# Performance work log

Hardware: AMD Instinct MI355X
Metric: run time of the kernel (lower is better)

The kernel has to match this reference:

```python
import jax, jax.numpy as jnp
import numpy as np

B, C, H, W = 4, 256, 128, 128
K = 3
BN = max(16, C // 4)  # 64
PAD = K // 2
EPS = 1e-5


def conv2d(x, w, b=None, pad=0):
    out = jax.lax.conv_general_dilated(
        x, w, (1, 1), [(pad, pad), (pad, pad)],
        dimension_numbers=("NCHW", "OIHW", "NCHW"))
    if b is not None:
        out = out + b[None, :, None, None]
    return out


def deform_conv2d(z, offset, mask, w, b):
    # torchvision modulated deform conv v2: offset [B,2*K*K,H,W] interleaved (dy,dx),
    # mask [B,K*K,H,W], kernel positions row-major, stride 1, pad PAD.
    Bz, Cb, Hz, Wz = z.shape
    K2 = K * K
    off = offset.reshape(Bz, K2, 2, Hz, Wz)
    ky, kx = jnp.meshgrid(jnp.arange(K), jnp.arange(K), indexing="ij")
    # sampling positions py/px: [B, K2, H, W]
    py = off[:, :, 0] + jnp.arange(Hz)[None, None, :, None] + (ky.reshape(K2) - PAD)[None, :, None, None]
    px = off[:, :, 1] + jnp.arange(Wz)[None, None, None, :] + (kx.reshape(K2) - PAD)[None, :, None, None]
    y0 = jnp.floor(py)
    x0 = jnp.floor(px)
    wy1 = py - y0  # frac weights
    wx1 = px - x0
    z_flat = z.reshape(Bz, Cb, Hz * Wz)

    def gather(yy, xx, wgt):
        valid = (yy >= 0) & (yy < Hz) & (xx >= 0) & (xx < Wz)
        yc = jnp.clip(yy, 0, Hz - 1).astype(jnp.int32)
        xc = jnp.clip(xx, 0, Wz - 1).astype(jnp.int32)
        idx = (yc * Wz + xc).reshape(Bz, K2 * Hz * Wz)
        g = jnp.take_along_axis(z_flat, idx[:, None, :], axis=2)  # [B, Cb, K2*H*W]
        g = g.reshape(Bz, Cb, K2, Hz, Wz)
        return g * (wgt * valid.astype(z.dtype))[:, None]

    val = (gather(y0, x0, (1 - wy1) * (1 - wx1))
           + gather(y0, x0 + 1, (1 - wy1) * wx1)
           + gather(y0 + 1, x0, wy1 * (1 - wx1))
           + gather(y0 + 1, x0 + 1, wy1 * wx1))
    val = val * mask[:, None]  # modulate: [B, Cb, K2, H, W]
    out = jnp.einsum("bckhw,ock->bohw", val, w.reshape(w.shape[0], Cb, K2))
    return out + b[None, :, None, None]


def setup_inputs() -> dict:
    key = jax.random.key(0)
    ks = jax.random.split(key, 11)
    s = 0.05
    return {
        "x": jax.random.normal(ks[0], (B, C, H, W), jnp.float32),
        "down_w": jax.random.normal(ks[1], (BN, C, 1, 1), jnp.float32) * s,
        "off_w": jax.random.normal(ks[2], (2 * K * K, BN, 3, 3), jnp.float32) * s,
        "off_b": jax.random.normal(ks[3], (2 * K * K,), jnp.float32) * s,
        "mask_w": jax.random.normal(ks[4], (K * K, BN, 3, 3), jnp.float32) * s,
        "mask_b": jax.random.normal(ks[5], (K * K,), jnp.float32) * s,
        "def_w": jax.random.normal(ks[6], (BN, BN, K, K), jnp.float32) * s,
        "def_b": jax.random.normal(ks[7], (BN,), jnp.float32) * s,
        "up_w": jax.random.normal(ks[8], (C, BN, 1, 1), jnp.float32) * s,
        "gamma": jnp.ones((C,), jnp.float32),
        "beta": jnp.zeros((C,), jnp.float32),
    }


def reference(x, down_w, off_w, off_b, mask_w, mask_b, def_w, def_b, up_w, gamma, beta):
    z = conv2d(x, down_w)                               # 1x1 down: [B, BN, H, W]
    offset = conv2d(z, off_w, off_b, pad=1)             # [B, 18, H, W]
    mask = jax.nn.sigmoid(conv2d(z, mask_w, mask_b, pad=1))  # [B, 9, H, W]
    z = deform_conv2d(z, offset, mask, def_w, def_b)    # [B, BN, H, W]
    z = conv2d(z, up_w)                                 # 1x1 up: [B, C, H, W]
    y = x + z
    # BatchNorm2d in training mode: batch statistics over (B, H, W), biased var
    mean = jnp.mean(y, axis=(0, 2, 3), keepdims=True)
    var = jnp.var(y, axis=(0, 2, 3), keepdims=True)
    yh = (y - mean) * jax.lax.rsqrt(var + EPS)
    yh = yh * gamma[None, :, None, None] + beta[None, :, None, None]
    return yh * jax.nn.sigmoid(yh)  # SiLU
```

## Files before the change

kernel.cpp:

```cpp
#include <hip/hip_runtime.h>
#include <hip/hip_bf16.h>


typedef __attribute__((ext_vector_type(8))) short bf16x8;
typedef __attribute__((ext_vector_type(4))) short bf16x4;
typedef __attribute__((ext_vector_type(4))) float f32x4;

#define HW   16384
#define CC   256
#define BNC  64

#define WS_STATS   0
#define WS_SS      262144
#define WS_FD      264192
#define WS_FOM     296960
#define WS_FDEF    333824
#define WS_FUP     407552
#define WS_ZBF     440320
#define WS_OM      8828928

__device__ __forceinline__ short f2b(float f) {
    unsigned u = __float_as_uint(f);
    unsigned r = (u + 0x7FFFu + ((u >> 16) & 1u)) >> 16;
    return (short)r;
}
__device__ __forceinline__ float b2f(short s) {
    return __uint_as_float(((unsigned)(unsigned short)s) << 16);
}

__global__ void k_prep(const float* __restrict__ down_w, const float* __restrict__ off_w,
                       const float* __restrict__ mask_w, const float* __restrict__ def_w,
                       const float* __restrict__ up_w, char* __restrict__ ws) {
    int g = blockIdx.x * 256 + threadIdx.x;
    int row = g >> 6, lane = g & 63;
    if (row >= 172) return;
    int l15 = lane & 15, q = lane >> 4;
    short vals[8];
    short* dst;
    if (row < 32) {
        int nt = row >> 3, kk = row & 7;
        int n = nt * 16 + l15;
        for (int j = 0; j < 8; ++j) {
            int c = kk * 32 + q * 8 + j;
            vals[j] = f2b(down_w[n * 256 + c]);
        }
        dst = (short*)(ws + WS_FD) + row * 512 + lane * 8;
    } else if (row < 68) {
        int r = row - 32; int nt = r / 18, kk = r % 18;
        int n = nt * 16 + l15;
        for (int j = 0; j < 8; ++j) {
            int kap = kk * 32 + q * 8 + j; int k = kap >> 6, c = kap & 63;
            float v = 0.f;
            if (n < 18)      v = off_w[(n * 64 + c) * 9 + k];
            else if (n < 27) v = mask_w[((n - 18) * 64 + c) * 9 + k];
            vals[j] = f2b(v);
        }
        dst = (short*)(ws + WS_FOM) + r * 512 + lane * 8;
    } else if (row < 140) {
        int r = row - 68; int nt = r / 18, kk = r % 18;
        int n = nt * 16 + l15;
        int u = kk * 4 + q, k = u >> 3;
        for (int j = 0; j < 8; ++j) {
            int c = (u & 7) * 8 + j;
            vals[j] = f2b(def_w[(n * 64 + c) * 9 + k]);
        }
        dst = (short*)(ws + WS_FDEF) + r * 512 + lane * 8;
    } else {
        int r = row - 140; int nt = r >> 1, kk = r & 1;
        int o = nt * 16 + l15;
        for (int j = 0; j < 8; ++j) {
            int c = kk * 32 + q * 8 + j;
            vals[j] = f2b(up_w[o * 64 + c]);
        }
        dst = (short*)(ws + WS_FUP) + r * 512 + lane * 8;
    }
    for (int j = 0; j < 8; ++j) dst[j] = vals[j];
}

__global__ __launch_bounds__(256) void k_down(const float* __restrict__ x,
                                              const short* __restrict__ wfd,
                                              short* __restrict__ zbf) {
    __shared__ __align__(16) short xl[64 * 264];
    int blk = blockIdx.x;
    int b = blk >> 8;
    int hw0 = (blk & 255) * 64;
    int t = threadIdx.x;
    const float* xb = x + (size_t)b * CC * HW + hw0;
    int px = t & 63, w = t >> 6;
    for (int h = 0; h < 8; ++h) {
        int c0 = h * 32 + w * 8;
        bf16x8 pk;
        #pragma unroll
        for (int j = 0; j < 8; ++j)
            pk[j] = f2b(xb[(size_t)(c0 + j) * HW + px]);
        *(bf16x8*)(&xl[px * 264 + c0]) = pk;
    }
    __syncthreads();
    int lane = t & 63, wv = t >> 6;
    int l15 = lane & 15, q = lane >> 4;
    bf16x8 A[8];
    const short* xrow = &xl[(wv * 16 + l15) * 264];
    for (int kk = 0; kk < 8; ++kk)
        A[kk] = *(const bf16x8*)(xrow + kk * 32 + q * 8);
    const bf16x8* Bp = (const bf16x8*)wfd;
    size_t obase = ((size_t)b * HW + hw0 + wv * 16) * 64;
    for (int nt = 0; nt < 4; ++nt) {
        f32x4 acc = {0.f, 0.f, 0.f, 0.f};
        for (int kk = 0; kk < 8; ++kk) {
            bf16x8 Bf = Bp[(nt * 8 + kk) * 64 + lane];
            acc = __builtin_amdgcn_mfma_f32_16x16x32_bf16(A[kk], Bf, acc, 0, 0, 0);
        }
        int n = nt * 16 + l15;
        for (int r = 0; r < 4; ++r) {
            int prow = q * 4 + r;
            zbf[obase + (size_t)prow * 64 + n] = f2b(acc[r]);
        }
    }
}

__global__ __launch_bounds__(256) void k_offmask(const short* __restrict__ zbf,
                                                 const short* __restrict__ wfom,
                                                 const float* __restrict__ off_b,
                                                 const float* __restrict__ mask_b,
                                                 float* __restrict__ om) {
    int blk = blockIdx.x;
    int b = blk >> 8;
    int hw0 = (blk & 255) * 64;
    int y = hw0 >> 7, x0 = hw0 & 127;
    int t = threadIdx.x, lane = t & 63, wv = t >> 6;
    int l15 = lane & 15, q = lane >> 4;
    int xx0 = x0 + wv * 16 + l15;
    const short* zb = zbf + (size_t)b * HW * 64;
    f32x4 acc0 = {0, 0, 0, 0}, acc1 = {0, 0, 0, 0};
    const bf16x8* Bp = (const bf16x8*)wfom;
    for (int kk = 0; kk < 18; ++kk) {
        int k = kk >> 1;
        int yy = y + (k / 3) - 1;
        int xx = xx0 + (k % 3) - 1;
        int c0 = (kk & 1) * 32 + q * 8;
        bf16x8 A = {0, 0, 0, 0, 0, 0, 0, 0};
        if (yy >= 0 && yy < 128 && xx >= 0 && xx < 128)
            A = *(const bf16x8*)(zb + ((size_t)(yy * 128 + xx)) * 64 + c0);
        bf16x8 B0 = Bp[kk * 64 + lane];
        bf16x8 B1 = Bp[(18 + kk) * 64 + lane];
        acc0 = __builtin_amdgcn_mfma_f32_16x16x32_bf16(A, B0, acc0, 0, 0, 0);
        acc1 = __builtin_amdgcn_mfma_f32_16x16x32_bf16(A, B1, acc1, 0, 0, 0);
    }
    float* omb = om + ((size_t)b * HW + hw0 + wv * 16) * 27;
    for (int half = 0; half < 2; ++half) {
        f32x4 acc = half ? acc1 : acc0;
        int n = half * 16 + l15;
        if (n < 27) {
            for (int r = 0; r < 4; ++r) {
                int prow = q * 4 + r;
                float v = acc[r];
                if (n < 18) v += off_b[n];
                else { v += mask_b[n - 18]; v = 1.f / (1.f + __expf(-v)); }
                omb[prow * 27 + n] = v;
            }
        }
    }
}

__global__ __launch_bounds__(256) void k_deform_up(
        const short* __restrict__ zbf, const float* __restrict__ om,
        const short* __restrict__ wfdef, const float* __restrict__ def_b,
        const short* __restrict__ wfup, const float* __restrict__ x,
        float* __restrict__ yout, float* __restrict__ stats) {
    __shared__ __align__(16) short valA[1152 * 8];
    __shared__ __align__(16) char  uSm[4608];
    int4*   pAi4 = (int4*)uSm;
    float4* pAw4 = (float4*)(uSm + 2304);
    short*  z2t  = (short*)uSm;

    int blk = blockIdx.x;
    int b = blk >> 10;
    int tile = blk & 1023;
    int oy = tile >> 3, xt = (tile & 7) << 4;
    int hw0 = oy * 128 + xt;
    int t = threadIdx.x;
    const short* zbs = zbf + (size_t)b * HW * 64;
    if (t < 144) {
        int px = t / 9, k = t % 9;
        int ox = xt + px;
        const float* p = om + ((size_t)b * HW + hw0 + px) * 27;
        float dy = p[2 * k], dx = p[2 * k + 1], m = p[18 + k];
        float py  = (float)oy + (float)(k / 3 - 1) + dy;
        float pxf = (float)ox + (float)(k % 3 - 1) + dx;
        float fy = floorf(py), fx = floorf(pxf);
        int iy = (int)fy, ix = (int)fx;
        float wy = py - fy, wx = pxf - fx;
        float ww[4] = { (1.f - wy) * (1.f - wx) * m, (1.f - wy) * wx * m,
                        wy * (1.f - wx) * m,          wy * wx * m };
        int ys[2] = {iy, iy + 1}, xs[2] = {ix, ix + 1};
        int   ri[4]; float rw[4];
        for (int ci = 0; ci < 4; ++ci) {
            int cy = ys[ci >> 1], cx = xs[ci & 1];
            bool v = (cy >= 0 && cy < 128 && cx >= 0 && cx < 128);
            ri[ci] = v ? (cy * 128 + cx) * 64 : 0;
            rw[ci] = v ? ww[ci] : 0.f;
        }
        pAi4[t] = make_int4(ri[0], ri[1], ri[2], ri[3]);
        pAw4[t] = make_float4(rw[0], rw[1], rw[2], rw[3]);
    }
    __syncthreads();
    for (int it = 0; it < 5; ++it) {
        int s = t + it * 256;
        if (s < 1152) {
            int px = s & 15, u = s >> 4;
            int k = u >> 3, cg = u & 7;
            int task = px * 9 + k;
            int4   idx = pAi4[task];
            float4 wt  = pAw4[task];
            int   ii[4] = { idx.x, idx.y, idx.z, idx.w };
            float wwt[4] = { wt.x, wt.y, wt.z, wt.w };
            int cgs = cg * 8;
            float acc[8] = {0.f, 0.f, 0.f, 0.f, 0.f, 0.f, 0.f, 0.f};
            #pragma unroll
            for (int ci = 0; ci < 4; ++ci) {
                float w = wwt[ci];
                int4 d = *(const int4*)(zbs + ii[ci] + cgs);
                int dp[4] = { d.x, d.y, d.z, d.w };
                #pragma unroll
                for (int p = 0; p < 4; ++p) {
                    float lo = __uint_as_float((unsigned)dp[p] << 16);
                    float hi = __uint_as_float((unsigned)dp[p] & 0xffff0000u);
                    acc[2 * p]     += w * lo;
                    acc[2 * p + 1] += w * hi;
                }
            }
            bf16x8 out;
            #pragma unroll
            for (int j = 0; j < 8; ++j) out[j] = f2b(acc[j]);
            *(bf16x8*)(&valA[s * 8]) = out;
        }
    }
    __syncthreads();
    int lane = t & 63, wv = t >> 6;
    int l15 = lane & 15, q = lane >> 4;
    {
        f32x4 acc = {0, 0, 0, 0};
        const bf16x8* Bp = (const bf16x8*)wfdef;
        const bf16x8* Ap = (const bf16x8*)valA;
        for (int kk = 0; kk < 18; ++kk) {
            bf16x8 A  = Ap[kk * 64 + lane];
            bf16x8 Bf = Bp[(wv * 18 + kk) * 64 + lane];
            acc = __builtin_amdgcn_mfma_f32_16x16x32_bf16(A, Bf, acc, 0, 0, 0);
        }
        int n = wv * 16 + l15;
        float bias = def_b[n];
        __syncthreads();
        for (int r = 0; r < 4; ++r) {
            int prow = q * 4 + r;
            z2t[prow * 64 + (n ^ ((prow & 7) << 3))] = f2b(acc[r] + bias);
        }
    }
    __syncthreads();
    int rsw = (l15 & 7) << 3;
    bf16x8 A0 = *(const bf16x8*)&z2t[l15 * 64 + ((q * 8) ^ rsw)];
    bf16x8 A1 = *(const bf16x8*)&z2t[l15 * 64 + ((32 + q * 8) ^ rsw)];
    const bf16x8* Bu = (const bf16x8*)wfup;
    int bucket = blk & 127;
    size_t xybase = (size_t)b * CC * HW + hw0 + q * 4;
    for (int nt = 0; nt < 4; ++nt) {
        int ont = wv * 4 + nt;
        f32x4 acc = {0, 0, 0, 0};
        acc = __builtin_amdgcn_mfma_f32_16x16x32_bf16(A0, Bu[(ont * 2 + 0) * 64 + lane], acc, 0, 0, 0);
        acc = __builtin_amdgcn_mfma_f32_16x16x32_bf16(A1, Bu[(ont * 2 + 1) * 64 + lane], acc, 0, 0, 0);
        int o = ont * 16 + l15;
        size_t pb = xybase + (size_t)o * HW;
        float4 xv = *(const float4*)(x + pb);
        float v0 = acc[0] + xv.x;
        float v1 = acc[1] + xv.y;
        float v2 = acc[2] + xv.z;
        float v3 = acc[3] + xv.w;
        *(float4*)(yout + pb) = make_float4(v0, v1, v2, v3);
        float s  = v0 + v1 + v2 + v3;
        float s2 = v0 * v0 + v1 * v1 + v2 * v2 + v3 * v3;
        s  += __shfl_xor(s, 16);  s  += __shfl_xor(s, 32);
        s2 += __shfl_xor(s2, 16); s2 += __shfl_xor(s2, 32);
        if (q == 0) {
            atomicAdd(&stats[bucket * 512 + o], s);
            atomicAdd(&stats[bucket * 512 + 256 + o], s2);
        }
    }
}

__global__ void k_stats(const float* __restrict__ stats, const float* __restrict__ gamma,
                        const float* __restrict__ beta, float* __restrict__ ss) {
    int o = threadIdx.x;
    float s = 0.f, s2 = 0.f;
    for (int u = 0; u < 128; ++u) { s += stats[u * 512 + o]; s2 += stats[u * 512 + 256 + o]; }
    float mean = s * (1.f / 65536.f);
    float var  = s2 * (1.f / 65536.f) - mean * mean;
    float rs = rsqrtf(var + 1e-5f);
    float sc = gamma[o] * rs;
    ss[o]       = sc;
    ss[256 + o] = beta[o] - mean * sc;
}

__global__ __launch_bounds__(256) void k_bn(float* __restrict__ y, const float* __restrict__ ss) {
    int g = blockIdx.x * 256 + threadIdx.x;
    int o = (g >> 10) & 255;
    float sc = ss[o], sh = ss[256 + o];
    float4* p = (float4*)y + (size_t)g * 4;
    for (int i = 0; i < 4; ++i) {
        float4 v = p[i];
        float vf[4] = { v.x, v.y, v.z, v.w };
        for (int j = 0; j < 4; ++j) {
            float h = vf[j] * sc + sh;
            vf[j] = h / (1.f + __expf(-h));
        }
        p[i] = make_float4(vf[0], vf[1], vf[2], vf[3]);
    }
}

extern "C" void kernel_launch(void* const* d_in, const int* in_sizes, int n_in,
                              void* d_out, int out_size, void* d_ws, size_t ws_size,
                              hipStream_t stream) {
    const float* x      = (const float*)d_in[0];
    const float* down_w = (const float*)d_in[1];
    const float* off_w  = (const float*)d_in[2];
    const float* off_b  = (const float*)d_in[3];
    const float* mask_w = (const float*)d_in[4];
    const float* mask_b = (const float*)d_in[5];
    const float* def_w  = (const float*)d_in[6];
    const float* def_b  = (const float*)d_in[7];
    const float* up_w   = (const float*)d_in[8];
    const float* gamma  = (const float*)d_in[9];
    const float* beta   = (const float*)d_in[10];
    char* ws = (char*)d_ws;
    float* stats = (float*)(ws + WS_STATS);
    float* ss    = (float*)(ws + WS_SS);
    short* wfd   = (short*)(ws + WS_FD);
    short* wfom  = (short*)(ws + WS_FOM);
    short* wfdef = (short*)(ws + WS_FDEF);
    short* wfup  = (short*)(ws + WS_FUP);
    short* zbf   = (short*)(ws + WS_ZBF);
    float* om    = (float*)(ws + WS_OM);
    float* y     = (float*)d_out;

    hipMemsetAsync(stats, 0, 128 * 512 * sizeof(float), stream);
    hipLaunchKernelGGL(k_prep,      dim3(43),   dim3(256), 0, stream, down_w, off_w, mask_w, def_w, up_w, ws);
    hipLaunchKernelGGL(k_down,      dim3(1024), dim3(256), 0, stream, x, wfd, zbf);
    hipLaunchKernelGGL(k_offmask,   dim3(1024), dim3(256), 0, stream, zbf, wfom, off_b, mask_b, om);
    hipLaunchKernelGGL(k_deform_up, dim3(4096), dim3(256), 0, stream, zbf, om, wfdef, def_b, wfup, x, y, stats);
    hipLaunchKernelGGL(k_stats,     dim3(1),    dim3(256), 0, stream, stats, gamma, beta, ss);
    hipLaunchKernelGGL(k_bn,        dim3(4096), dim3(256), 0, stream, y, ss);
}
```

Baseline: 246.3 us.

## Prefetch residual x early, batch gather loads, packed bf16 cvt, unroll stats reduce

The deform+up kernel now loads its residual x values at kernel start so that the global latency overlaps the offset and gather phases. The bilinear gather issues eight 16-byte loads per iteration before computing, uses packed f32x2 FMAs and the v_cvt_pk_bf16_f32 instruction, and sets launch bounds to 4 blocks per unit. A redundant barrier is removed, and the stats reduction uses four independent accumulators. Holding x in registers raises register pressure, and the occupancy hint may force spills.

```diff
diff --git a/kernel.cpp b/kernel.cpp
--- a/kernel.cpp
+++ b/kernel.cpp
@@ -5,6 +5,7 @@
 typedef __attribute__((ext_vector_type(8))) short bf16x8;
 typedef __attribute__((ext_vector_type(4))) short bf16x4;
 typedef __attribute__((ext_vector_type(4))) float f32x4;
+typedef __attribute__((ext_vector_type(2))) float f32x2;
 
 #define HW   16384
 #define CC   256
@@ -26,6 +27,30 @@
 }
 __device__ __forceinline__ float b2f(short s) {
     return __uint_as_float(((unsigned)(unsigned short)s) << 16);
+}
+
+__device__ __forceinline__ void bilin_acc(f32x2 acc[4], int4 d, float w) {
+    f32x2 w2 = {w, w};
+    int dp[4] = {d.x, d.y, d.z, d.w};
+    #pragma unroll
+    for (int p = 0; p < 4; ++p) {
+        f32x2 v;
+        v.x = __uint_as_float((unsigned)dp[p] << 16);
+        v.y = __uint_as_float((unsigned)dp[p] & 0xffff0000u);
+        acc[p] += w2 * v;
+    }
+}
+__device__ __forceinline__ void bilin_store(short* dst, int4 d0, int4 d1,
+                                            int4 d2, int4 d3, float4 wt) {
+    f32x2 acc[4] = {{0.f,0.f},{0.f,0.f},{0.f,0.f},{0.f,0.f}};
+    bilin_acc(acc, d0, wt.x); bilin_acc(acc, d1, wt.y);
+    bilin_acc(acc, d2, wt.z); bilin_acc(acc, d3, wt.w);
+    unsigned r0, r1, r2, r3;
+    asm("v_cvt_pk_bf16_f32 %0, %1, %2" : "=v"(r0) : "v"(acc[0].x), "v"(acc[0].y));
+    asm("v_cvt_pk_bf16_f32 %0, %1, %2" : "=v"(r1) : "v"(acc[1].x), "v"(acc[1].y));
+    asm("v_cvt_pk_bf16_f32 %0, %1, %2" : "=v"(r2) : "v"(acc[2].x), "v"(acc[2].y));
+    asm("v_cvt_pk_bf16_f32 %0, %1, %2" : "=v"(r3) : "v"(acc[3].x), "v"(acc[3].y));
+    *(int4*)dst = make_int4((int)r0, (int)r1, (int)r2, (int)r3);
 }
 
 __global__ void k_prep(const float* __restrict__ down_w, const float* __restrict__ off_w,
@@ -162,7 +187,7 @@
     }
 }
 
-__global__ __launch_bounds__(256) void k_deform_up(
+__global__ __launch_bounds__(256, 4) void k_deform_up(
         const short* __restrict__ zbf, const float* __restrict__ om,
         const short* __restrict__ wfdef, const float* __restrict__ def_b,
         const short* __restrict__ wfup, const float* __restrict__ x,
@@ -179,7 +204,18 @@
     int oy = tile >> 3, xt = (tile & 7) << 4;
     int hw0 = oy * 128 + xt;
     int t = threadIdx.x;
+    int lane = t & 63, wv = t >> 6;
+    int l15 = lane & 15, q = lane >> 4;
     const short* zbs = zbf + (size_t)b * HW * 64;
+
+    size_t xybase = (size_t)b * CC * HW + hw0 + q * 4;
+    float4 xv[4];
+    #pragma unroll
+    for (int nt = 0; nt < 4; ++nt) {
+        int o = (wv * 4 + nt) * 16 + l15;
+        xv[nt] = *(const float4*)(x + xybase + (size_t)o * HW);
+    }
+
     if (t < 144) {
         int px = t / 9, k = t % 9;
         int ox = xt + px;
@@ -204,40 +240,40 @@
         pAw4[t] = make_float4(rw[0], rw[1], rw[2], rw[3]);
     }
     __syncthreads();
-    for (int it = 0; it < 5; ++it) {
-        int s = t + it * 256;
-        if (s < 1152) {
-            int px = s & 15, u = s >> 4;
-            int k = u >> 3, cg = u & 7;
-            int task = px * 9 + k;
-            int4   idx = pAi4[task];
-            float4 wt  = pAw4[task];
-            int   ii[4] = { idx.x, idx.y, idx.z, idx.w };
-            float wwt[4] = { wt.x, wt.y, wt.z, wt.w };
-            int cgs = cg * 8;
-            float acc[8] = {0.f, 0.f, 0.f, 0.f, 0.f, 0.f, 0.f, 0.f};
-            #pragma unroll
-            for (int ci = 0; ci < 4; ++ci) {
-                float w = wwt[ci];
-                int4 d = *(const int4*)(zbs + ii[ci] + cgs);
-                int dp[4] = { d.x, d.y, d.z, d.w };
-                #pragma unroll
-                for (int p = 0; p < 4; ++p) {
-                    float lo = __uint_as_float((unsigned)dp[p] << 16);
-                    float hi = __uint_as_float((unsigned)dp[p] & 0xffff0000u);
-                    acc[2 * p]     += w * lo;
-                    acc[2 * p + 1] += w * hi;
-                }
-            }
-            bf16x8 out;
-            #pragma unroll
-            for (int j = 0; j < 8; ++j) out[j] = f2b(acc[j]);
-            *(bf16x8*)(&valA[s * 8]) = out;
-        }
+    #pragma unroll
+    for (int it = 0; it < 2; ++it) {
+        int s0 = t + it * 512, s1 = s0 + 256;
+        int px0 = s0 & 15, u0 = s0 >> 4;
+        int px1 = s1 & 15, u1 = s1 >> 4;
+        int4   ia = pAi4[px0 * 9 + (u0 >> 3)];
+        float4 wa = pAw4[px0 * 9 + (u0 >> 3)];
+        int4   ib = pAi4[px1 * 9 + (u1 >> 3)];
+        float4 wb = pAw4[px1 * 9 + (u1 >> 3)];
+        int ca = (u0 & 7) * 8, cb = (u1 & 7) * 8;
+        int4 da0 = *(const int4*)(zbs + ia.x + ca);
+        int4 da1 = *(const int4*)(zbs + ia.y + ca);
+        int4 da2 = *(const int4*)(zbs + ia.z + ca);
+        int4 da3 = *(const int4*)(zbs + ia.w + ca);
+        int4 db0 = *(const int4*)(zbs + ib.x + cb);
+        int4 db1 = *(const int4*)(zbs + ib.y + cb);
+        int4 db2 = *(const int4*)(zbs + ib.z + cb);
+        int4 db3 = *(const int4*)(zbs + ib.w + cb);
+        bilin_store(&valA[s0 * 8], da0, da1, da2, da3, wa);
+        bilin_store(&valA[s1 * 8], db0, db1, db2, db3, wb);
+    }
+    if (t < 128) {
+        int s = 1024 + t;
+        int px = s & 15, u = s >> 4;
+        int4   ia = pAi4[px * 9 + (u >> 3)];
+        float4 wa = pAw4[px * 9 + (u >> 3)];
+        int ca = (u & 7) * 8;
+        int4 d0 = *(const int4*)(zbs + ia.x + ca);
+        int4 d1 = *(const int4*)(zbs + ia.y + ca);
+        int4 d2 = *(const int4*)(zbs + ia.z + ca);
+        int4 d3 = *(const int4*)(zbs + ia.w + ca);
+        bilin_store(&valA[s * 8], d0, d1, d2, d3, wa);
     }
     __syncthreads();
-    int lane = t & 63, wv = t >> 6;
-    int l15 = lane & 15, q = lane >> 4;
     {
         f32x4 acc = {0, 0, 0, 0};
         const bf16x8* Bp = (const bf16x8*)wfdef;
@@ -249,7 +285,6 @@
         }
         int n = wv * 16 + l15;
         float bias = def_b[n];
-        __syncthreads();
         for (int r = 0; r < 4; ++r) {
             int prow = q * 4 + r;
             z2t[prow * 64 + (n ^ ((prow & 7) << 3))] = f2b(acc[r] + bias);
@@ -261,7 +296,7 @@
     bf16x8 A1 = *(const bf16x8*)&z2t[l15 * 64 + ((32 + q * 8) ^ rsw)];
     const bf16x8* Bu = (const bf16x8*)wfup;
     int bucket = blk & 127;
-    size_t xybase = (size_t)b * CC * HW + hw0 + q * 4;
+    #pragma unroll
     for (int nt = 0; nt < 4; ++nt) {
         int ont = wv * 4 + nt;
         f32x4 acc = {0, 0, 0, 0};
@@ -269,11 +304,10 @@
         acc = __builtin_amdgcn_mfma_f32_16x16x32_bf16(A1, Bu[(ont * 2 + 1) * 64 + lane], acc, 0, 0, 0);
         int o = ont * 16 + l15;
         size_t pb = xybase + (size_t)o * HW;
-        float4 xv = *(const float4*)(x + pb);
-        float v0 = acc[0] + xv.x;
-        float v1 = acc[1] + xv.y;
-        float v2 = acc[2] + xv.z;
-        float v3 = acc[3] + xv.w;
+        float v0 = acc[0] + xv[nt].x;
+        float v1 = acc[1] + xv[nt].y;
+        float v2 = acc[2] + xv[nt].z;
+        float v3 = acc[3] + xv[nt].w;
         *(float4*)(yout + pb) = make_float4(v0, v1, v2, v3);
         float s  = v0 + v1 + v2 + v3;
         float s2 = v0 * v0 + v1 * v1 + v2 * v2 + v3 * v3;
@@ -289,8 +323,17 @@
 __global__ void k_stats(const float* __restrict__ stats, const float* __restrict__ gamma,
                         const float* __restrict__ beta, float* __restrict__ ss) {
     int o = threadIdx.x;
-    float s = 0.f, s2 = 0.f;
-    for (int u = 0; u < 128; ++u) { s += stats[u * 512 + o]; s2 += stats[u * 512 + 256 + o]; }
+    float a0 = 0.f, a1 = 0.f, a2 = 0.f, a3 = 0.f;
+    float b0 = 0.f, b1 = 0.f, b2 = 0.f, b3 = 0.f;
+    #pragma unroll 4
+    for (int u = 0; u < 128; u += 4) {
+        a0 += stats[(u + 0) * 512 + o];  b0 += stats[(u + 0) * 512 + 256 + o];
+        a1 += stats[(u + 1) * 512 + o];  b1 += stats[(u + 1) * 512 + 256 + o];
+        a2 += stats[(u + 2) * 512 + o];  b2 += stats[(u + 2) * 512 + 256 + o];
+        a3 += stats[(u + 3) * 512 + o];  b3 += stats[(u + 3) * 512 + 256 + o];
+    }
+    float s = (a0 + a1) + (a2 + a3);
+    float s2 = (b0 + b1) + (b2 + b3);
     float mean = s * (1.f / 65536.f);
     float var  = s2 * (1.f / 65536.f) - mean * mean;
     float rs = rsqrtf(var + 1e-5f);
```

Result: slower. 253.1 us (+2.8%).
